# Kernel optimization log

Hardware: AMD Instinct MI355X
Metric: run time of the kernel (lower is better)

Reference implementation:

```python
import jax, jax.numpy as jnp
import numpy as np

B, S, D = 1, 2048, 1024          # batch, seq, n_embd
E, F = 16, 1024                  # n_routed_experts, moe_intermediate_size
NG, TKG, K = 4, 2, 4             # n_group, topk_group, num_experts_per_tok
NSH = 2                          # n_shared_experts
SCALE = 2.5                      # routed_scaling_factor
STD = 0.02
EPG = E // NG                    # experts per group


def setup_inputs() -> dict:
    key = jax.random.key(0)
    ks = jax.random.split(key, 8)
    return {
        "hidden_states": jax.random.normal(ks[0], (B, S, D), jnp.float32),
        "router_w": jax.random.normal(ks[1], (E, D), jnp.float32) * STD,   # gate.weight
        "bias": jnp.zeros((E,), jnp.float32),                              # e_score_correction_bias
        "gate_w": jax.random.normal(ks[2], (E, D, F), jnp.float32) * STD,  # per-expert gate_proj (transposed)
        "up_w": jax.random.normal(ks[3], (E, D, F), jnp.float32) * STD,    # per-expert up_proj
        "down_w": jax.random.normal(ks[4], (E, F, D), jnp.float32) * STD,  # per-expert down_proj
        "sh_gate_w": jax.random.normal(ks[5], (D, NSH * F), jnp.float32) * STD,
        "sh_up_w": jax.random.normal(ks[6], (D, NSH * F), jnp.float32) * STD,
        "sh_down_w": jax.random.normal(ks[7], (NSH * F, D), jnp.float32) * STD,
    }


def _route(x_flat, router_w, bias):
    # x_flat: [T, D] -> topk_idx [T, K], topk_w [T, K]
    logits = x_flat.astype(jnp.float32) @ router_w.T          # [T, E]
    scores = jax.nn.sigmoid(logits)
    s = scores + bias[None, :]                                # scores_for_choice
    sg = s.reshape(-1, NG, EPG)
    group_score = jax.lax.top_k(sg, 2)[0].sum(-1)             # sum of top-2 per group [T, NG]
    gidx = jax.lax.top_k(group_score, TKG)[1]                 # [T, TKG]
    gmask = jnp.sum(jax.nn.one_hot(gidx, NG, dtype=jnp.float32), axis=1) > 0   # [T, NG]
    emask = jnp.repeat(gmask, EPG, axis=1)                    # [T, E]
    masked = jnp.where(emask, s, -1.0)
    topk_idx = jax.lax.top_k(masked, K)[1]                    # [T, K]
    tw = jnp.take_along_axis(scores, topk_idx, axis=1)        # gather raw sigmoid scores
    tw = tw / (tw.sum(-1, keepdims=True) + 1e-20)             # norm_topk_prob
    tw = tw * SCALE
    return topk_idx, tw


def reference(hidden_states, router_w, bias, gate_w, up_w, down_w,
              sh_gate_w, sh_up_w, sh_down_w):
    x = hidden_states.reshape(-1, D)                          # [T, D]
    topk_idx, tw = _route(x, router_w, bias)
    # combine weights per (token, expert): scatter-add of topk weights
    combine = (jax.nn.one_hot(topk_idx, E, dtype=tw.dtype) * tw[..., None]).sum(1)  # [T, E]
    # per-expert SwiGLU MLPs (dense dispatch, masked combine == index_add semantics)
    h = jnp.einsum('td,edf->etf', x, gate_w)                  # [E, T, F]
    u = jnp.einsum('td,edf->etf', x, up_w)
    y = jnp.einsum('etf,efd->etd', jax.nn.silu(h) * u, down_w)  # [E, T, D]
    routed = jnp.einsum('etd,te->td', y, combine)             # weighted combine
    # shared experts
    sh = (jax.nn.silu(x @ sh_gate_w) * (x @ sh_up_w)) @ sh_down_w
    return (routed + sh).reshape(hidden_states.shape)
```

## Files before the change

kernel.cpp:

```cpp
#include <hip/hip_runtime.h>
#include <cstdint>
#include <cstddef>


#define T_TOK 2048
#define DIM   1024
#define NEXP  16
#define FDIM  1024
#define MAXTILES 80
#define MAXSLOTS (MAXTILES*128)

typedef __bf16 bf16x8_t __attribute__((ext_vector_type(8)));
typedef float  f32x4_t  __attribute__((ext_vector_type(4)));
typedef unsigned short ushort8_t __attribute__((ext_vector_type(8)));
typedef unsigned short ushort4_t __attribute__((ext_vector_type(4)));

#define OFF_XB     (0UL)
#define OFF_GATET  (4UL<<20)
#define OFF_UPT    (36UL<<20)
#define OFF_DOWNT  (68UL<<20)
#define OFF_SHGT   (100UL<<20)
#define OFF_SHUT   (104UL<<20)
#define OFF_SHDT   (108UL<<20)
#define OFF_H      (112UL<<20)
#define OFF_U      (132UL<<20)
#define OFF_YSLOT  (152UL<<20)
#define OFF_CTRL   (172UL<<20)
#define CT_OFFSETS  128
#define CT_NTILES   192
#define CT_TILEEXP  256
#define CT_SLOTTOK  4096
#define CT_TKSLOT   49152
#define CT_TOPKIDX  81920
#define CT_TOPKW    114688

__device__ __forceinline__ unsigned short f2bf(float f) {
  __bf16 h = (__bf16)f;
  return __builtin_bit_cast(unsigned short, h);
}
__device__ __forceinline__ float bf2f(unsigned short u) {
  unsigned int v = ((unsigned int)u) << 16;
  return __builtin_bit_cast(float, v);
}
__device__ __forceinline__ void gld16(const void* g, void* l) {
  __builtin_amdgcn_global_load_lds(
      (const __attribute__((address_space(1))) void*)(g),
      (__attribute__((address_space(3))) void*)(l), 16, 0, 0);
}

__global__ void k_cvt(const float* __restrict__ src, unsigned short* __restrict__ dst, int n4) {
  int i = blockIdx.x * blockDim.x + threadIdx.x;
  if (i >= n4) return;
  float4 v = ((const float4*)src)[i];
  ushort4_t o;
  o[0] = f2bf(v.x); o[1] = f2bf(v.y); o[2] = f2bf(v.z); o[3] = f2bf(v.w);
  ((ushort4_t*)dst)[i] = o;
}

__global__ void k_transpose(const float* __restrict__ src, unsigned short* __restrict__ dst,
                            int R, int C) {
  __shared__ unsigned short tile[64 * 68];
  long b = blockIdx.z;
  src += b * (long)R * C;
  dst += b * (long)R * C;
  int cT = blockIdx.x * 64, rT = blockIdx.y * 64;
  int t = threadIdx.x;
  int rb = t >> 4, cb = t & 15;
  float f[4][4];
#pragma unroll
  for (int i = 0; i < 4; i++) {
    float4 v = *(const float4*)(src + (long)(rT + 4 * rb + i) * C + cT + 4 * cb);
    f[i][0] = v.x; f[i][1] = v.y; f[i][2] = v.z; f[i][3] = v.w;
  }
#pragma unroll
  for (int j = 0; j < 4; j++) {
    ushort4_t o;
    o[0] = f2bf(f[0][j]); o[1] = f2bf(f[1][j]); o[2] = f2bf(f[2][j]); o[3] = f2bf(f[3][j]);
    int c = 4 * cb + j;
    *(ushort4_t*)&tile[c * 68 + 4 * rb] = o;
  }
  __syncthreads();
#pragma unroll
  for (int p = 0; p < 2; p++) {
    int q = t + 256 * p;
    int c = q >> 3, r0 = (q & 7) * 8;
    ushort4_t lo = *(const ushort4_t*)&tile[c * 68 + r0];
    ushort4_t hi = *(const ushort4_t*)&tile[c * 68 + r0 + 4];
    ushort8_t w8 = {lo[0], lo[1], lo[2], lo[3], hi[0], hi[1], hi[2], hi[3]};
    *(ushort8_t*)(dst + (long)(cT + c) * R + rT + r0) = w8;
  }
}

__global__ __launch_bounds__(256) void k_router(
    const float* __restrict__ x, const float* __restrict__ rw,
    const float* __restrict__ bias, int* __restrict__ topk_idx,
    float* __restrict__ topk_w) {
  int t = blockIdx.x, tid = threadIdx.x;
  int wv = tid >> 6, lane = tid & 63;
  float4 xv = ((const float4*)(x + (size_t)t * DIM))[tid];
  float part[NEXP];
#pragma unroll
  for (int e = 0; e < NEXP; e++) {
    float4 wr = ((const float4*)(rw + (size_t)e * DIM))[tid];
    part[e] = xv.x * wr.x + xv.y * wr.y + xv.z * wr.z + xv.w * wr.w;
  }
  __shared__ float wsum_s[4 * NEXP];
#pragma unroll
  for (int e = 0; e < NEXP; e++) {
    float v = part[e];
#pragma unroll
    for (int off = 32; off; off >>= 1) v += __shfl_xor(v, off, 64);
    if (lane == 0) wsum_s[wv * NEXP + e] = v;
  }
  __syncthreads();
  if (tid == 0) {
    float r_sc[NEXP], r_s[NEXP];
#pragma unroll
    for (int e = 0; e < NEXP; e++) {
      float logit = wsum_s[e] + wsum_s[NEXP + e] + wsum_s[2 * NEXP + e] +
                    wsum_s[3 * NEXP + e];
      float sc = 1.f / (1.f + expf(-logit));
      r_sc[e] = sc;
      r_s[e] = sc + bias[e];
    }
    float gs[4];
#pragma unroll
    for (int g = 0; g < 4; g++) {
      float m1 = -1e30f, m2 = -1e30f;
#pragma unroll
      for (int j = 0; j < 4; j++) {
        float v = r_s[g * 4 + j];
        if (v > m1) { m2 = m1; m1 = v; } else if (v > m2) m2 = v;
      }
      gs[g] = m1 + m2;
    }
    int g1 = 0;
    for (int g = 1; g < 4; g++) if (gs[g] > gs[g1]) g1 = g;
    int g2 = -1;
    for (int g = 0; g < 4; g++) { if (g == g1) continue; if (g2 < 0 || gs[g] > gs[g2]) g2 = g; }
    int taken = 0, idx[4];
    float w[4], wsum = 1e-20f;
#pragma unroll
    for (int k = 0; k < 4; k++) {
      float best = -1e30f; int bi = 0;
#pragma unroll
      for (int e2 = 0; e2 < 16; e2++) {
        if (taken & (1 << e2)) continue;
        int g = e2 >> 2;
        float v = (g == g1 || g == g2) ? r_s[e2] : -1.f;
        if (v > best) { best = v; bi = e2; }
      }
      taken |= 1 << bi; idx[k] = bi;
    }
#pragma unroll
    for (int k = 0; k < 4; k++) { w[k] = r_sc[idx[k]]; wsum += w[k]; }
    float sc2 = 2.5f / wsum;
#pragma unroll
    for (int k = 0; k < 4; k++) {
      topk_idx[t * 4 + k] = idx[k];
      topk_w[t * 4 + k] = w[k] * sc2;
    }
  }
}

__global__ __launch_bounds__(256) void k_route_post(
    const int* __restrict__ topk_idx, int* __restrict__ offsets,
    int* __restrict__ tile_expert, int* __restrict__ n_tiles,
    int* __restrict__ slot_token, int* __restrict__ tk_slot) {
  __shared__ int cnt[NEXP][257];
  __shared__ int offs[NEXP], tot[NEXP], s_ntiles;
  int tid = threadIdx.x;
  int4 ent[8];
#pragma unroll
  for (int i = 0; i < 8; i++) ent[i] = ((const int4*)topk_idx)[tid * 8 + i];
  int lc[NEXP];
#pragma unroll
  for (int j = 0; j < NEXP; j++) lc[j] = 0;
#pragma unroll
  for (int i = 0; i < 8; i++) {
    int es[4] = {ent[i].x, ent[i].y, ent[i].z, ent[i].w};
#pragma unroll
    for (int k = 0; k < 4; k++)
#pragma unroll
      for (int j = 0; j < NEXP; j++) lc[j] += (es[k] == j) ? 1 : 0;
  }
#pragma unroll
  for (int j = 0; j < NEXP; j++) cnt[j][tid] = lc[j];
  __syncthreads();
  if (tid < NEXP) {
    int base = 0;
    for (int c = 0; c < 256; c += 8) {
      int v[8];
#pragma unroll
      for (int i = 0; i < 8; i++) v[i] = cnt[tid][c + i];
#pragma unroll
      for (int i = 0; i < 8; i++) { cnt[tid][c + i] = base; base += v[i]; }
    }
    tot[tid] = base;
  }
  __syncthreads();
  if (tid == 0) {
    int cum = 0, tt = 0;
    for (int e = 0; e < NEXP; e++) {
      offs[e] = cum;
      offsets[e] = cum;
      int nt = (tot[e] + 127) >> 7;
      for (int i = 0; i < nt; i++) tile_expert[tt++] = e;
      cum += nt << 7;
    }
    n_tiles[0] = tt;
    s_ntiles = tt;
  }
  __syncthreads();
  for (int e = 0; e < NEXP; e++) {
    int s0 = offs[e] + tot[e];
    int s1 = offs[e] + (((tot[e] + 127) >> 7) << 7);
    for (int s = s0 + tid; s < s1; s += 256) slot_token[s] = -1;
  }
  int lcur[NEXP];
#pragma unroll
  for (int j = 0; j < NEXP; j++) lcur[j] = offs[j] + cnt[j][tid];
#pragma unroll
  for (int i = 0; i < 8; i++) {
    int t = tid * 8 + i;
    int es[4] = {ent[i].x, ent[i].y, ent[i].z, ent[i].w};
#pragma unroll
    for (int k = 0; k < 4; k++) {
      int e = es[k], pos = 0;
#pragma unroll
      for (int j = 0; j < NEXP; j++) pos += (e == j) ? lcur[j] : 0;
#pragma unroll
      for (int j = 0; j < NEXP; j++) lcur[j] += (e == j) ? 1 : 0;
      slot_token[pos] = t;
      tk_slot[t * 4 + k] = pos;
    }
  }
}

template <int MODE>
__global__ __launch_bounds__(256) void k_gemm(
    const unsigned short* __restrict__ Abase, const unsigned short* __restrict__ B0,
    const unsigned short* __restrict__ B1, unsigned short* __restrict__ O0,
    unsigned short* __restrict__ O1, float* __restrict__ OF,
    const int* __restrict__ slot_token, const int* __restrict__ tile_expert,
    const int* __restrict__ n_tiles) {
  constexpr int KT = (MODE == 3) ? 64 : 32;
  constexpr int AW = (MODE == 3) ? 2048 : 1024;
  constexpr int BW = (MODE == 3) ? 2048 : 1024;
  int bx = blockIdx.x, by = blockIdx.y;
  if (MODE == 0 || MODE == 1) { if (bx >= n_tiles[0]) return; }
  const unsigned short* Bp;
  int n0;
  if (MODE == 0) { int e = tile_expert[bx]; Bp = (by < 8 ? B0 : B1) + (size_t)e * 1024 * 1024; n0 = (by & 7) * 128; }
  else if (MODE == 1) { int e = tile_expert[bx]; Bp = B0 + (size_t)e * 1024 * 1024; n0 = by * 128; }
  else if (MODE == 2) { Bp = (by < 16 ? B0 : B1); n0 = (by & 15) * 128; }
  else { Bp = B0; n0 = by * 128; }

  __shared__ unsigned short sA[128 * 32];
  __shared__ unsigned short sB[128 * 32];

  int tid = threadIdx.x;
  int w = tid >> 6, L = tid & 63;
  int c0 = w * 128 + L, c1 = c0 + 64;
  int ar0 = c0 >> 2, ar1 = c1 >> 2;
  long arow0, arow1;
  if (MODE == 0) {
    int t0 = slot_token[bx * 128 + ar0]; if (t0 < 0) t0 = 0;
    int t1 = slot_token[bx * 128 + ar1]; if (t1 < 0) t1 = 0;
    arow0 = t0; arow1 = t1;
  } else {
    arow0 = bx * 128 + ar0; arow1 = bx * 128 + ar1;
  }
  const char* aA = (const char*)(Abase + arow0 * AW) + (c0 & 3) * 16;
  const char* aB = (const char*)(Abase + arow1 * AW) + (c1 & 3) * 16;
  const char* bA = (const char*)(Bp + (size_t)(n0 + ar0) * BW) + (c0 & 3) * 16;
  const char* bB = (const char*)(Bp + (size_t)(n0 + ar1) * BW) + (c1 & 3) * 16;
  char* sAu0 = (char*)sA + (w * 128) * 16;
  char* sAu1 = (char*)sA + (w * 128 + 64) * 16;
  char* sBu0 = (char*)sB + (w * 128) * 16;
  char* sBu1 = (char*)sB + (w * 128 + 64) * 16;

  f32x4_t acc[4][4];
#pragma unroll
  for (int i = 0; i < 4; i++)
#pragma unroll
    for (int j = 0; j < 4; j++) acc[i][j] = f32x4_t{0.f, 0.f, 0.f, 0.f};

  int mb = (w >> 1) * 64, nb = (w & 1) * 64;
  int lr = L & 15, k8 = (L >> 4) * 8;

  for (int kt = 0; kt < KT; ++kt) {
    gld16(aA, sAu0); gld16(aB, sAu1);
    gld16(bA, sBu0); gld16(bB, sBu1);
    aA += 64; aB += 64; bA += 64; bB += 64;
    __syncthreads();
    bf16x8_t af[4], bfv[4];
#pragma unroll
    for (int i = 0; i < 4; i++) af[i] = *(const bf16x8_t*)(sA + (mb + 16 * i + lr) * 32 + k8);
#pragma unroll
    for (int i = 0; i < 4; i++) bfv[i] = *(const bf16x8_t*)(sB + (nb + 16 * i + lr) * 32 + k8);
#pragma unroll
    for (int i = 0; i < 4; i++)
#pragma unroll
      for (int j = 0; j < 4; j++)
        acc[i][j] = __builtin_amdgcn_mfma_f32_16x16x32_bf16(af[i], bfv[j], acc[i][j], 0, 0, 0);
    __syncthreads();
  }

  int quad = L >> 4;
#pragma unroll
  for (int i = 0; i < 4; i++) {
    int rowb = bx * 128 + mb + 16 * i + quad * 4;
#pragma unroll
    for (int j = 0; j < 4; j++) {
      int col = n0 + nb + 16 * j + lr;
#pragma unroll
      for (int r = 0; r < 4; r++) {
        float v = acc[i][j][r];
        if (MODE == 0) (by < 8 ? O0 : O1)[(size_t)(rowb + r) * 1024 + col] = f2bf(v);
        else if (MODE == 1) O0[(size_t)(rowb + r) * 1024 + col] = f2bf(v);
        else if (MODE == 2) (by < 16 ? O0 : O1)[(size_t)(rowb + r) * 2048 + col] = f2bf(v);
        else OF[(size_t)(rowb + r) * 1024 + col] = v;
      }
    }
  }
}

__global__ void k_silu_mul(const unsigned short* h, const unsigned short* u,
                           unsigned short* o, int n4) {
  int i = blockIdx.x * blockDim.x + threadIdx.x;
  if (i >= n4) return;
  ushort4_t hv = ((const ushort4_t*)h)[i];
  ushort4_t uv = ((const ushort4_t*)u)[i];
  ushort4_t ov;
#pragma unroll
  for (int j = 0; j < 4; j++) {
    float hf = bf2f(hv[j]);
    float uf = bf2f(uv[j]);
    ov[j] = f2bf(hf / (1.f + expf(-hf)) * uf);
  }
  ((ushort4_t*)o)[i] = ov;
}

__global__ void k_gather(float* __restrict__ out, const unsigned short* __restrict__ yslot,
                         const int* __restrict__ tk_slot, const float* __restrict__ topk_w) {
  int t = blockIdx.x, tid = threadIdx.x;
  int4 sl = ((const int4*)tk_slot)[t];
  float4 wv = ((const float4*)topk_w)[t];
  int d = 4 * tid;
  float4 o = *(float4*)(out + (size_t)t * 1024 + d);
  const int s[4] = {sl.x, sl.y, sl.z, sl.w};
  const float wk[4] = {wv.x, wv.y, wv.z, wv.w};
#pragma unroll
  for (int k = 0; k < 4; k++) {
    ushort4_t y = *(const ushort4_t*)(yslot + (size_t)s[k] * 1024 + d);
    o.x += wk[k] * bf2f(y[0]);
    o.y += wk[k] * bf2f(y[1]);
    o.z += wk[k] * bf2f(y[2]);
    o.w += wk[k] * bf2f(y[3]);
  }
  *(float4*)(out + (size_t)t * 1024 + d) = o;
}

extern "C" void kernel_launch(void* const* d_in, const int* in_sizes, int n_in,
                              void* d_out, int out_size, void* d_ws, size_t ws_size,
                              hipStream_t stream) {
  const float* x = (const float*)d_in[0];
  const float* rw = (const float*)d_in[1];
  const float* bias = (const float*)d_in[2];
  const float* gw = (const float*)d_in[3];
  const float* uw = (const float*)d_in[4];
  const float* dw = (const float*)d_in[5];
  const float* sg = (const float*)d_in[6];
  const float* su = (const float*)d_in[7];
  const float* sd = (const float*)d_in[8];
  float* out = (float*)d_out;
  char* ws = (char*)d_ws;

  unsigned short* xb    = (unsigned short*)(ws + OFF_XB);
  unsigned short* gateT = (unsigned short*)(ws + OFF_GATET);
  unsigned short* upT   = (unsigned short*)(ws + OFF_UPT);
  unsigned short* downT = (unsigned short*)(ws + OFF_DOWNT);
  unsigned short* shGT  = (unsigned short*)(ws + OFF_SHGT);
  unsigned short* shUT  = (unsigned short*)(ws + OFF_SHUT);
  unsigned short* shDT  = (unsigned short*)(ws + OFF_SHDT);
  unsigned short* Hbuf  = (unsigned short*)(ws + OFF_H);
  unsigned short* Ubuf  = (unsigned short*)(ws + OFF_U);
  unsigned short* yslot = (unsigned short*)(ws + OFF_YSLOT);
  char* ctrl = ws + OFF_CTRL;
  int* offsets_    = (int*)(ctrl + CT_OFFSETS);
  int* n_tiles     = (int*)(ctrl + CT_NTILES);
  int* tile_expert = (int*)(ctrl + CT_TILEEXP);
  int* slot_token  = (int*)(ctrl + CT_SLOTTOK);
  int* tk_slot     = (int*)(ctrl + CT_TKSLOT);
  int* topk_idx    = (int*)(ctrl + CT_TOPKIDX);
  float* topk_w    = (float*)(ctrl + CT_TOPKW);

  k_cvt<<<2048, 256, 0, stream>>>(x, xb, T_TOK * DIM / 4);
  k_transpose<<<dim3(16, 16, 16), 256, 0, stream>>>(gw, gateT, 1024, 1024);
  k_transpose<<<dim3(16, 16, 16), 256, 0, stream>>>(uw, upT, 1024, 1024);
  k_transpose<<<dim3(16, 16, 16), 256, 0, stream>>>(dw, downT, 1024, 1024);
  k_transpose<<<dim3(32, 16, 1), 256, 0, stream>>>(sg, shGT, 1024, 2048);
  k_transpose<<<dim3(32, 16, 1), 256, 0, stream>>>(su, shUT, 1024, 2048);
  k_transpose<<<dim3(16, 32, 1), 256, 0, stream>>>(sd, shDT, 2048, 1024);
  k_router<<<2048, 256, 0, stream>>>(x, rw, bias, topk_idx, topk_w);
  k_route_post<<<1, 256, 0, stream>>>(topk_idx, offsets_, tile_expert, n_tiles,
                                      slot_token, tk_slot);
  k_gemm<0><<<dim3(MAXTILES, 16), 256, 0, stream>>>(xb, gateT, upT, Hbuf, Ubuf, nullptr,
                                                    slot_token, tile_expert, n_tiles);
  k_silu_mul<<<MAXSLOTS, 256, 0, stream>>>(Hbuf, Ubuf, Hbuf, MAXSLOTS * 1024 / 4);
  k_gemm<1><<<dim3(MAXTILES, 8), 256, 0, stream>>>(Hbuf, downT, nullptr, yslot, nullptr, nullptr,
                                                   slot_token, tile_expert, n_tiles);
  k_gemm<2><<<dim3(16, 32), 256, 0, stream>>>(xb, shGT, shUT, Hbuf, Ubuf, nullptr,
                                              slot_token, tile_expert, n_tiles);
  k_silu_mul<<<4096, 256, 0, stream>>>(Hbuf, Ubuf, Hbuf, T_TOK * 2048 / 4);
  k_gemm<3><<<dim3(16, 8), 256, 0, stream>>>(Hbuf, shDT, nullptr, nullptr, nullptr, out,
                                             slot_token, tile_expert, n_tiles);
  k_gather<<<2048, 256, 0, stream>>>(out, yslot, tk_slot, topk_w);
}
```

Before: 491.8 us.

## Fuse SiLU-mul into gate/up GEMMs, swizzle LDS, split-K shared down GEMM

Gate and up projections now run in one GEMM kernel with two accumulator sets, and the SiLU*mul epilogue is applied in registers. This removes the separate silu_mul kernels and the round trip of the H/U intermediates through global memory. The LDS layout gets an XOR swizzle to cut bank conflicts, and the grid is reordered so N-tiles vary fastest, which should improve reuse of the A tile. The shared down-projection is split-K into two partial fp32 buffers that the gather kernel sums. The cost is higher register pressure from the doubled accumulators, only partly offset by the launch_bounds occupancy hint, plus extra partial-buffer traffic.

New measurement: 475.3 us. 3.4% less time.

```diff
diff --git a/kernel.cpp b/kernel.cpp
--- a/kernel.cpp
+++ b/kernel.cpp
@@ -168,7 +168,7 @@
     int* __restrict__ tile_expert, int* __restrict__ n_tiles,
     int* __restrict__ slot_token, int* __restrict__ tk_slot) {
   __shared__ int cnt[NEXP][257];
-  __shared__ int offs[NEXP], tot[NEXP], s_ntiles;
+  __shared__ int offs[NEXP], tot[NEXP];
   int tid = threadIdx.x;
   int4 ent[8];
 #pragma unroll
@@ -209,7 +209,6 @@
       cum += nt << 7;
     }
     n_tiles[0] = tt;
-    s_ntiles = tt;
   }
   __syncthreads();
   for (int e = 0; e < NEXP; e++) {
@@ -238,117 +237,131 @@
 }
 
 template <int MODE>
-__global__ __launch_bounds__(256) void k_gemm(
+__global__ __launch_bounds__(256, 2) void k_gemm(
     const unsigned short* __restrict__ Abase, const unsigned short* __restrict__ B0,
     const unsigned short* __restrict__ B1, unsigned short* __restrict__ O0,
-    unsigned short* __restrict__ O1, float* __restrict__ OF,
+    float* __restrict__ OF,
     const int* __restrict__ slot_token, const int* __restrict__ tile_expert,
     const int* __restrict__ n_tiles) {
-  constexpr int KT = (MODE == 3) ? 64 : 32;
+  constexpr bool FUSED = (MODE == 0 || MODE == 2);
+  constexpr int KT = (MODE == 3) ? 32 : 32;
   constexpr int AW = (MODE == 3) ? 2048 : 1024;
   constexpr int BW = (MODE == 3) ? 2048 : 1024;
-  int bx = blockIdx.x, by = blockIdx.y;
-  if (MODE == 0 || MODE == 1) { if (bx >= n_tiles[0]) return; }
-  const unsigned short* Bp;
-  int n0;
-  if (MODE == 0) { int e = tile_expert[bx]; Bp = (by < 8 ? B0 : B1) + (size_t)e * 1024 * 1024; n0 = (by & 7) * 128; }
-  else if (MODE == 1) { int e = tile_expert[bx]; Bp = B0 + (size_t)e * 1024 * 1024; n0 = by * 128; }
-  else if (MODE == 2) { Bp = (by < 16 ? B0 : B1); n0 = (by & 15) * 128; }
-  else { Bp = B0; n0 = by * 128; }
+  constexpr int OW = (MODE == 2) ? 2048 : 1024;
+
+  int nx = blockIdx.x, bt = blockIdx.y;
+  if (MODE == 0 || MODE == 1) { if (bt >= n_tiles[0]) return; }
+  int n0 = nx * 128;
+  const unsigned short *Bg, *Bu = nullptr;
+  if (MODE == 0) { int e = tile_expert[bt]; Bg = B0 + (size_t)e * 1024 * 1024; Bu = B1 + (size_t)e * 1024 * 1024; }
+  else if (MODE == 1) { int e = tile_expert[bt]; Bg = B0 + (size_t)e * 1024 * 1024; }
+  else if (MODE == 2) { Bg = B0; Bu = B1; }
+  else { Bg = B0; }
 
   __shared__ unsigned short sA[128 * 32];
-  __shared__ unsigned short sB[128 * 32];
+  __shared__ unsigned short sBg[128 * 32];
+  __shared__ unsigned short sBu[FUSED ? 128 * 32 : 1];
 
   int tid = threadIdx.x;
   int w = tid >> 6, L = tid & 63;
   int c0 = w * 128 + L, c1 = c0 + 64;
   int ar0 = c0 >> 2, ar1 = c1 >> 2;
+  int ch0 = (c0 & 3) ^ (ar0 & 3), ch1 = (c1 & 3) ^ (ar1 & 3);
   long arow0, arow1;
   if (MODE == 0) {
-    int t0 = slot_token[bx * 128 + ar0]; if (t0 < 0) t0 = 0;
-    int t1 = slot_token[bx * 128 + ar1]; if (t1 < 0) t1 = 0;
+    int t0 = slot_token[bt * 128 + ar0]; if (t0 < 0) t0 = 0;
+    int t1 = slot_token[bt * 128 + ar1]; if (t1 < 0) t1 = 0;
     arow0 = t0; arow1 = t1;
   } else {
-    arow0 = bx * 128 + ar0; arow1 = bx * 128 + ar1;
-  }
-  const char* aA = (const char*)(Abase + arow0 * AW) + (c0 & 3) * 16;
-  const char* aB = (const char*)(Abase + arow1 * AW) + (c1 & 3) * 16;
-  const char* bA = (const char*)(Bp + (size_t)(n0 + ar0) * BW) + (c0 & 3) * 16;
-  const char* bB = (const char*)(Bp + (size_t)(n0 + ar1) * BW) + (c1 & 3) * 16;
-  char* sAu0 = (char*)sA + (w * 128) * 16;
-  char* sAu1 = (char*)sA + (w * 128 + 64) * 16;
-  char* sBu0 = (char*)sB + (w * 128) * 16;
-  char* sBu1 = (char*)sB + (w * 128 + 64) * 16;
-
-  f32x4_t acc[4][4];
+    arow0 = bt * 128 + ar0; arow1 = bt * 128 + ar1;
+  }
+  long kbase = (MODE == 3) ? (long)blockIdx.z * 1024 : 0;
+  const char* aA = (const char*)(Abase + arow0 * AW + kbase) + ch0 * 16;
+  const char* aB = (const char*)(Abase + arow1 * AW + kbase) + ch1 * 16;
+  const char* gA = (const char*)(Bg + (size_t)(n0 + ar0) * BW + kbase) + ch0 * 16;
+  const char* gB = (const char*)(Bg + (size_t)(n0 + ar1) * BW + kbase) + ch1 * 16;
+  const char* uA = FUSED ? (const char*)(Bu + (size_t)(n0 + ar0) * BW) + ch0 * 16 : nullptr;
+  const char* uB = FUSED ? (const char*)(Bu + (size_t)(n0 + ar1) * BW) + ch1 * 16 : nullptr;
+  char* dA0 = (char*)sA + (w * 128) * 16;
+  char* dA1 = (char*)sA + (w * 128 + 64) * 16;
+  char* dG0 = (char*)sBg + (w * 128) * 16;
+  char* dG1 = (char*)sBg + (w * 128 + 64) * 16;
+  char* dU0 = (char*)sBu + (w * 128) * 16;
+  char* dU1 = (char*)sBu + (w * 128 + 64) * 16;
+
+  f32x4_t accg[4][4], accu[4][4];
 #pragma unroll
   for (int i = 0; i < 4; i++)
 #pragma unroll
-    for (int j = 0; j < 4; j++) acc[i][j] = f32x4_t{0.f, 0.f, 0.f, 0.f};
+    for (int j = 0; j < 4; j++) {
+      accg[i][j] = f32x4_t{0.f, 0.f, 0.f, 0.f};
+      if (FUSED) accu[i][j] = f32x4_t{0.f, 0.f, 0.f, 0.f};
+    }
 
   int mb = (w >> 1) * 64, nb = (w & 1) * 64;
-  int lr = L & 15, k8 = (L >> 4) * 8;
+  int lr = L & 15, quad = L >> 4;
+  int sw = ((quad ^ (lr & 3)) << 3);
 
   for (int kt = 0; kt < KT; ++kt) {
-    gld16(aA, sAu0); gld16(aB, sAu1);
-    gld16(bA, sBu0); gld16(bB, sBu1);
-    aA += 64; aB += 64; bA += 64; bB += 64;
+    gld16(aA, dA0); gld16(aB, dA1);
+    gld16(gA, dG0); gld16(gB, dG1);
+    if (FUSED) { gld16(uA, dU0); gld16(uB, dU1); }
+    aA += 64; aB += 64; gA += 64; gB += 64;
+    if (FUSED) { uA += 64; uB += 64; }
     __syncthreads();
-    bf16x8_t af[4], bfv[4];
-#pragma unroll
-    for (int i = 0; i < 4; i++) af[i] = *(const bf16x8_t*)(sA + (mb + 16 * i + lr) * 32 + k8);
-#pragma unroll
-    for (int i = 0; i < 4; i++) bfv[i] = *(const bf16x8_t*)(sB + (nb + 16 * i + lr) * 32 + k8);
+    bf16x8_t af[4], bg[4], bu[4];
+#pragma unroll
+    for (int i = 0; i < 4; i++) af[i] = *(const bf16x8_t*)(sA + (mb + 16 * i + lr) * 32 + sw);
+#pragma unroll
+    for (int i = 0; i < 4; i++) bg[i] = *(const bf16x8_t*)(sBg + (nb + 16 * i + lr) * 32 + sw);
+    if (FUSED) {
+#pragma unroll
+      for (int i = 0; i < 4; i++) bu[i] = *(const bf16x8_t*)(sBu + (nb + 16 * i + lr) * 32 + sw);
+    }
 #pragma unroll
     for (int i = 0; i < 4; i++)
 #pragma unroll
-      for (int j = 0; j < 4; j++)
-        acc[i][j] = __builtin_amdgcn_mfma_f32_16x16x32_bf16(af[i], bfv[j], acc[i][j], 0, 0, 0);
+      for (int j = 0; j < 4; j++) {
+        accg[i][j] = __builtin_amdgcn_mfma_f32_16x16x32_bf16(af[i], bg[j], accg[i][j], 0, 0, 0);
+        if (FUSED)
+          accu[i][j] = __builtin_amdgcn_mfma_f32_16x16x32_bf16(af[i], bu[j], accu[i][j], 0, 0, 0);
+      }
     __syncthreads();
   }
 
-  int quad = L >> 4;
 #pragma unroll
   for (int i = 0; i < 4; i++) {
-    int rowb = bx * 128 + mb + 16 * i + quad * 4;
+    int rowb = bt * 128 + mb + 16 * i + quad * 4;
 #pragma unroll
     for (int j = 0; j < 4; j++) {
       int col = n0 + nb + 16 * j + lr;
 #pragma unroll
       for (int r = 0; r < 4; r++) {
-        float v = acc[i][j][r];
-        if (MODE == 0) (by < 8 ? O0 : O1)[(size_t)(rowb + r) * 1024 + col] = f2bf(v);
-        else if (MODE == 1) O0[(size_t)(rowb + r) * 1024 + col] = f2bf(v);
-        else if (MODE == 2) (by < 16 ? O0 : O1)[(size_t)(rowb + r) * 2048 + col] = f2bf(v);
-        else OF[(size_t)(rowb + r) * 1024 + col] = v;
+        float h = accg[i][j][r];
+        if (FUSED) {
+          float u = accu[i][j][r];
+          float act = h / (1.f + __expf(-h)) * u;
+          O0[(size_t)(rowb + r) * OW + col] = f2bf(act);
+        } else if (MODE == 1) {
+          O0[(size_t)(rowb + r) * OW + col] = f2bf(h);
+        } else {
+          OF[(size_t)blockIdx.z * (T_TOK * 1024) + (size_t)(rowb + r) * 1024 + col] = h;
+        }
       }
     }
   }
 }
 
-__global__ void k_silu_mul(const unsigned short* h, const unsigned short* u,
-                           unsigned short* o, int n4) {
-  int i = blockIdx.x * blockDim.x + threadIdx.x;
-  if (i >= n4) return;
-  ushort4_t hv = ((const ushort4_t*)h)[i];
-  ushort4_t uv = ((const ushort4_t*)u)[i];
-  ushort4_t ov;
-#pragma unroll
-  for (int j = 0; j < 4; j++) {
-    float hf = bf2f(hv[j]);
-    float uf = bf2f(uv[j]);
-    ov[j] = f2bf(hf / (1.f + expf(-hf)) * uf);
-  }
-  ((ushort4_t*)o)[i] = ov;
-}
-
-__global__ void k_gather(float* __restrict__ out, const unsigned short* __restrict__ yslot,
+__global__ void k_gather(float* __restrict__ out, const float* __restrict__ partial,
+                         const unsigned short* __restrict__ yslot,
                          const int* __restrict__ tk_slot, const float* __restrict__ topk_w) {
   int t = blockIdx.x, tid = threadIdx.x;
   int4 sl = ((const int4*)tk_slot)[t];
   float4 wv = ((const float4*)topk_w)[t];
   int d = 4 * tid;
-  float4 o = *(float4*)(out + (size_t)t * 1024 + d);
+  float4 p0 = *(const float4*)(partial + (size_t)t * 1024 + d);
+  float4 p1 = *(const float4*)(partial + (size_t)(T_TOK * 1024) + (size_t)t * 1024 + d);
+  float4 o = {p0.x + p1.x, p0.y + p1.y, p0.z + p1.z, p0.w + p1.w};
   const int s[4] = {sl.x, sl.y, sl.z, sl.w};
   const float wk[4] = {wv.x, wv.y, wv.z, wv.w};
 #pragma unroll
@@ -385,7 +398,7 @@
   unsigned short* shUT  = (unsigned short*)(ws + OFF_SHUT);
   unsigned short* shDT  = (unsigned short*)(ws + OFF_SHDT);
   unsigned short* Hbuf  = (unsigned short*)(ws + OFF_H);
-  unsigned short* Ubuf  = (unsigned short*)(ws + OFF_U);
+  float*          part  = (float*)(ws + OFF_U);
   unsigned short* yslot = (unsigned short*)(ws + OFF_YSLOT);
   char* ctrl = ws + OFF_CTRL;
   int* offsets_    = (int*)(ctrl + CT_OFFSETS);
@@ -406,15 +419,13 @@
   k_router<<<2048, 256, 0, stream>>>(x, rw, bias, topk_idx, topk_w);
   k_route_post<<<1, 256, 0, stream>>>(topk_idx, offsets_, tile_expert, n_tiles,
                                       slot_token, tk_slot);
-  k_gemm<0><<<dim3(MAXTILES, 16), 256, 0, stream>>>(xb, gateT, upT, Hbuf, Ubuf, nullptr,
-                                                    slot_token, tile_expert, n_tiles);
-  k_silu_mul<<<MAXSLOTS, 256, 0, stream>>>(Hbuf, Ubuf, Hbuf, MAXSLOTS * 1024 / 4);
-  k_gemm<1><<<dim3(MAXTILES, 8), 256, 0, stream>>>(Hbuf, downT, nullptr, yslot, nullptr, nullptr,
+  k_gemm<0><<<dim3(8, MAXTILES), 256, 0, stream>>>(xb, gateT, upT, Hbuf, nullptr,
                                                    slot_token, tile_expert, n_tiles);
-  k_gemm<2><<<dim3(16, 32), 256, 0, stream>>>(xb, shGT, shUT, Hbuf, Ubuf, nullptr,
+  k_gemm<1><<<dim3(8, MAXTILES), 256, 0, stream>>>(Hbuf, downT, nullptr, yslot, nullptr,
+                                                   slot_token, tile_expert, n_tiles);
+  k_gemm<2><<<dim3(16, 16), 256, 0, stream>>>(xb, shGT, shUT, Hbuf, nullptr,
                                               slot_token, tile_expert, n_tiles);
-  k_silu_mul<<<4096, 256, 0, stream>>>(Hbuf, Ubuf, Hbuf, T_TOK * 2048 / 4);
-  k_gemm<3><<<dim3(16, 8), 256, 0, stream>>>(Hbuf, shDT, nullptr, nullptr, nullptr, out,
-                                             slot_token, tile_expert, n_tiles);
-  k_gather<<<2048, 256, 0, stream>>>(out, yslot, tk_slot, topk_w);
-}
+  k_gemm<3><<<dim3(8, 16, 2), 256, 0, stream>>>(Hbuf, shDT, nullptr, nullptr, part,
+                                                slot_token, tile_expert, n_tiles);
+  k_gather<<<2048, 256, 0, stream>>>(out, part, yslot, tk_slot, topk_w);
+}
```
